# Kernel tuning notes

Measured on AMD Instinct MI355X. Metric: run time of the kernel, lower is better.

Reference implementation:

```python
import jax, jax.numpy as jnp
import numpy as np
from math import sqrt

D_MODEL = 512
HEADS = 8
D_K = D_MODEL // HEADS
DIM_FFN = 2048
EPS = 1e-6


def setup_inputs() -> dict:
    key = jax.random.key(0)
    ks = jax.random.split(key, 16)
    b, s = 2, 256
    inp = {
        "x": jax.random.normal(ks[0], (b, s, D_MODEL), dtype=jnp.float32),
        "connection_bias_k": jax.random.normal(ks[1], (b, s, s, D_MODEL), dtype=jnp.float32) * 0.02,
        "connection_bias_v": jax.random.normal(ks[2], (b, s, s, D_MODEL), dtype=jnp.float32) * 0.02,
        "mask": jnp.zeros((b, s), dtype=jnp.int32),
        "Wq": jax.random.normal(ks[3], (D_MODEL, D_MODEL), dtype=jnp.float32) / sqrt(D_MODEL),
        "bq": jnp.zeros((D_MODEL,), dtype=jnp.float32),
        "Wk": jax.random.normal(ks[4], (D_MODEL, D_MODEL), dtype=jnp.float32) / sqrt(D_MODEL),
        "bk": jnp.zeros((D_MODEL,), dtype=jnp.float32),
        "Wv": jax.random.normal(ks[5], (D_MODEL, D_MODEL), dtype=jnp.float32) / sqrt(D_MODEL),
        "bv": jnp.zeros((D_MODEL,), dtype=jnp.float32),
        "Wo": jax.random.normal(ks[6], (D_MODEL, D_MODEL), dtype=jnp.float32) / sqrt(D_MODEL),
        "bo": jnp.zeros((D_MODEL,), dtype=jnp.float32),
        "alpha1": jnp.ones((D_MODEL,), dtype=jnp.float32),
        "beta1": jnp.zeros((D_MODEL,), dtype=jnp.float32),
        "alpha2": jnp.ones((D_MODEL,), dtype=jnp.float32),
        "beta2": jnp.zeros((D_MODEL,), dtype=jnp.float32),
        "W1": jax.random.normal(ks[7], (DIM_FFN, D_MODEL), dtype=jnp.float32) / sqrt(D_MODEL),
        "b1": jnp.zeros((DIM_FFN,), dtype=jnp.float32),
        "W2": jax.random.normal(ks[8], (D_MODEL, DIM_FFN), dtype=jnp.float32) / sqrt(DIM_FFN),
        "b2": jnp.zeros((D_MODEL,), dtype=jnp.float32),
    }
    return inp


def _norm(x, alpha, beta):
    # torch .std() is unbiased (ddof=1); note std is added to eps OUTSIDE variance
    mu = jnp.mean(x, axis=-1, keepdims=True)
    sd = jnp.std(x, axis=-1, ddof=1, keepdims=True)
    return alpha * (x - mu) / (sd + EPS) + beta


def reference(x, connection_bias_k, connection_bias_v, mask,
              Wq, bq, Wk, bk, Wv, bv, Wo, bo,
              alpha1, beta1, alpha2, beta2, W1, b1, W2, b2):
    b, s, _ = x.shape
    h, dk = HEADS, D_K

    x2 = _norm(x, alpha1, beta1)
    # projections -> [b, h, s, dk]
    q = (x2 @ Wq.T + bq).reshape(b, s, h, dk).transpose(0, 2, 1, 3)
    k = (x2 @ Wk.T + bk).reshape(b, s, h, dk).transpose(0, 2, 1, 3)
    v = (x2 @ Wv.T + bv).reshape(b, s, h, dk).transpose(0, 2, 1, 3)

    # biases reshaped to (b, s1, s2, h, dk); biased_k[b,h,i,j] = k[b,h,j] + bias[b,j,i,h]
    bk_r = connection_bias_k.reshape(b, s, s, h, dk)
    bv_r = connection_bias_v.reshape(b, s, s, h, dk)

    # scores[b,h,i,j] = q_i . (k_j + bias_k[b,j,i,h]) / sqrt(dk)
    scores = (jnp.einsum('bhid,bhjd->bhij', q, k)
              + jnp.einsum('bhid,bjihd->bhij', q, bk_r)) / sqrt(dk)

    # mask [b,s] -> [b,1,s,1], broadcast over heads and key dim (matches torch)
    m = mask[:, None, :, None]
    scores = jnp.where(m == 1, -1e9, scores)
    attn = jax.nn.softmax(scores, axis=-1)

    # out[b,h,i,d] = sum_j attn[b,h,i,j] * (v[b,h,j] + bias_v[b,j,i,h])
    out = (jnp.einsum('bhij,bhjd->bhid', attn, v)
           + jnp.einsum('bhij,bjihd->bhid', attn, bv_r))
    concat = out.transpose(0, 2, 1, 3).reshape(b, s, D_MODEL)
    attn_out = concat @ Wo.T + bo

    x = x + attn_out
    x2 = _norm(x, alpha2, beta2)
    ff = jax.nn.relu(x2 @ W1.T + b1) @ W2.T + b2
    return x + ff
```

## Files before the change

### kernel.cpp

```cpp
#include <hip/hip_runtime.h>
#include <math.h>

#define D_MODEL 512
#define NHEADS 8
#define DK 64
#define DFFN 2048

typedef __attribute__((ext_vector_type(8))) __bf16 bf16x8;
typedef __attribute__((ext_vector_type(4))) float floatx4;

__global__ __launch_bounds__(256) void ln_kernel(
    const float* __restrict__ x, const float* __restrict__ alpha,
    const float* __restrict__ beta, __bf16* __restrict__ y) {
  int row = blockIdx.x;
  int t = threadIdx.x;
  const float* xr = x + (size_t)row * D_MODEL;
  float2 v = ((const float2*)xr)[t];
  __shared__ float rs[256], rq[256];
  rs[t] = v.x + v.y;
  rq[t] = v.x * v.x + v.y * v.y;
  __syncthreads();
  for (int o = 128; o > 0; o >>= 1) {
    if (t < o) { rs[t] += rs[t + o]; rq[t] += rq[t + o]; }
    __syncthreads();
  }
  float mu = rs[0] * (1.0f / D_MODEL);
  float var = (rq[0] - (float)D_MODEL * mu * mu) * (1.0f / (D_MODEL - 1));
  float inv = 1.0f / (sqrtf(fmaxf(var, 0.0f)) + 1e-6f);
  float2 a2 = ((const float2*)alpha)[t];
  float2 b2 = ((const float2*)beta)[t];
  union { __bf16 h2[2]; unsigned int u; } pk;
  pk.h2[0] = (__bf16)(a2.x * (v.x - mu) * inv + b2.x);
  pk.h2[1] = (__bf16)(a2.y * (v.y - mu) * inv + b2.y);
  *(unsigned int*)(y + (size_t)row * D_MODEL + 2 * t) = pk.u;
}

struct Seg { const float* src; __bf16* dst; int n4; };
struct Segs6 { Seg s[6]; };
__global__ __launch_bounds__(256) void cast6(Segs6 cs) {
  Seg sg = cs.s[blockIdx.y];
  int stride = gridDim.x * 256;
  for (int idx = blockIdx.x * 256 + threadIdx.x; idx < sg.n4; idx += stride) {
    float4 f = ((const float4*)sg.src)[idx];
    union { __bf16 h[4]; uint2 u; } pk;
    pk.h[0] = (__bf16)f.x; pk.h[1] = (__bf16)f.y;
    pk.h[2] = (__bf16)f.z; pk.h[3] = (__bf16)f.w;
    ((uint2*)sg.dst)[idx] = pk.u;
  }
}

__global__ __launch_bounds__(256) void pack_bias(
    const float* __restrict__ bq, const float* __restrict__ bk,
    const float* __restrict__ bv, float* __restrict__ dst) {
  int idx = blockIdx.x * 256 + threadIdx.x;
  if (idx >= 3 * D_MODEL) return;
  float v = idx < 512 ? bq[idx] : (idx < 1024 ? bk[idx - 512] : bv[idx - 1024]);
  dst[idx] = v;
}

template <int RELU, int OUT_BF16>
__global__ __launch_bounds__(64) void wave_gemm(
    const __bf16* __restrict__ A, int lda, const __bf16* __restrict__ B, int ldb,
    const float* __restrict__ bias, const float* __restrict__ res,
    void* __restrict__ Cv, int N, int K) {
  int lane = threadIdx.x;
  int r16 = lane & 15;
  int ko = (lane >> 4) * 8;
  int m0 = blockIdx.y * 32, n0 = blockIdx.x * 32;
  const __bf16* A0 = A + (size_t)(m0 + r16) * lda + ko;
  const __bf16* A1 = A0 + (size_t)16 * lda;
  const __bf16* B0 = B + (size_t)(n0 + r16) * ldb + ko;
  const __bf16* B1 = B0 + (size_t)16 * ldb;
  floatx4 acc00 = {0.f, 0.f, 0.f, 0.f};
  floatx4 acc01 = acc00, acc10 = acc00, acc11 = acc00;
#pragma unroll 4
  for (int k0 = 0; k0 < K; k0 += 32) {
    bf16x8 a0 = *(const bf16x8*)(A0 + k0);
    bf16x8 a1 = *(const bf16x8*)(A1 + k0);
    bf16x8 b0 = *(const bf16x8*)(B0 + k0);
    bf16x8 b1 = *(const bf16x8*)(B1 + k0);
    acc00 = __builtin_amdgcn_mfma_f32_16x16x32_bf16(a0, b0, acc00, 0, 0, 0);
    acc01 = __builtin_amdgcn_mfma_f32_16x16x32_bf16(a0, b1, acc01, 0, 0, 0);
    acc10 = __builtin_amdgcn_mfma_f32_16x16x32_bf16(a1, b0, acc10, 0, 0, 0);
    acc11 = __builtin_amdgcn_mfma_f32_16x16x32_bf16(a1, b1, acc11, 0, 0, 0);
  }
  int col = lane & 15, rb = (lane >> 4) * 4;
  floatx4 accs[2][2] = {{acc00, acc01}, {acc10, acc11}};
#pragma unroll
  for (int i = 0; i < 2; ++i) {
#pragma unroll
    for (int j = 0; j < 2; ++j) {
#pragma unroll
      for (int r = 0; r < 4; ++r) {
        int row = m0 + i * 16 + rb + r;
        int cc = n0 + j * 16 + col;
        float v = accs[i][j][r] + bias[cc];
        if (res) v += res[(size_t)row * N + cc];
        if (RELU) v = fmaxf(v, 0.0f);
        if (OUT_BF16)
          ((__bf16*)Cv)[(size_t)row * N + cc] = (__bf16)v;
        else
          ((float*)Cv)[(size_t)row * N + cc] = v;
      }
    }
  }
}

__global__ __launch_bounds__(256) void attn_kernel(
    const float* __restrict__ qkv, int ldq,
    const float* __restrict__ cbk, const float* __restrict__ cbv,
    const int* __restrict__ mask, __bf16* __restrict__ concat, int s) {
  int i = blockIdx.x % s;
  int b = blockIdx.x / s;
  int t = threadIdx.x;
  int w = t >> 6;
  int lane = t & 63;
  int h = lane >> 3;

  __shared__ float sc[NHEADS][257];
  __shared__ float sums[NHEADS];
  __shared__ float part[4][D_MODEL];

  size_t tok_i = (size_t)(b * s + i);
  const float* qp = qkv + tok_i * ldq + lane * 8;
  float4 q0 = *(const float4*)(qp);
  float4 q1 = *(const float4*)(qp + 4);

  for (int jj = 0; jj < 64; ++jj) {
    int j = w * 64 + jj;
    size_t tok_j = (size_t)(b * s + j);
    const float* kp = qkv + tok_j * ldq + 512 + lane * 8;
    const float* cp = cbk + (tok_j * s + i) * D_MODEL + lane * 8;
    float4 k0 = *(const float4*)(kp);
    float4 k1 = *(const float4*)(kp + 4);
    float4 c0 = *(const float4*)(cp);
    float4 c1 = *(const float4*)(cp + 4);
    float d = q0.x * (k0.x + c0.x) + q0.y * (k0.y + c0.y) +
              q0.z * (k0.z + c0.z) + q0.w * (k0.w + c0.w) +
              q1.x * (k1.x + c1.x) + q1.y * (k1.y + c1.y) +
              q1.z * (k1.z + c1.z) + q1.w * (k1.w + c1.w);
    d += __shfl_xor(d, 1);
    d += __shfl_xor(d, 2);
    d += __shfl_xor(d, 4);
    if ((lane & 7) == 0) sc[h][j] = d * 0.125f;
  }
  __syncthreads();

  {
    int hh = 2 * w + (lane >> 5);
    int l32 = lane & 31;
    bool masked = (mask[b * s + i] == 1);
    float vals[8];
    float mx = -1e30f;
#pragma unroll
    for (int kk = 0; kk < 8; ++kk) {
      float xv = sc[hh][l32 + kk * 32];
      if (masked) xv = -1e9f;
      vals[kk] = xv;
      mx = fmaxf(mx, xv);
    }
    for (int m = 1; m < 32; m <<= 1) mx = fmaxf(mx, __shfl_xor(mx, m, 32));
    float ls = 0.f;
#pragma unroll
    for (int kk = 0; kk < 8; ++kk) {
      float e = expf(vals[kk] - mx);
      sc[hh][l32 + kk * 32] = e;
      ls += e;
    }
    for (int m = 1; m < 32; m <<= 1) ls += __shfl_xor(ls, m, 32);
    if (l32 == 0) sums[hh] = ls;
  }
  __syncthreads();

  float4 a0 = {0.f, 0.f, 0.f, 0.f};
  float4 a1 = {0.f, 0.f, 0.f, 0.f};
  for (int jj = 0; jj < 64; ++jj) {
    int j = w * 64 + jj;
    size_t tok_j = (size_t)(b * s + j);
    const float* vp = qkv + tok_j * ldq + 1024 + lane * 8;
    const float* cp = cbv + (tok_j * s + i) * D_MODEL + lane * 8;
    float4 v0 = *(const float4*)(vp);
    float4 v1 = *(const float4*)(vp + 4);
    float4 c0 = *(const float4*)(cp);
    float4 c1 = *(const float4*)(cp + 4);
    float pj = sc[h][j];
    a0.x += pj * (v0.x + c0.x); a0.y += pj * (v0.y + c0.y);
    a0.z += pj * (v0.z + c0.z); a0.w += pj * (v0.w + c0.w);
    a1.x += pj * (v1.x + c1.x); a1.y += pj * (v1.y + c1.y);
    a1.z += pj * (v1.z + c1.z); a1.w += pj * (v1.w + c1.w);
  }
  *(float4*)&part[w][lane * 8] = a0;
  *(float4*)&part[w][lane * 8 + 4] = a1;
  __syncthreads();

  int d0 = t * 2;
  float inv = 1.0f / sums[d0 >> 6];
  float o0 = (part[0][d0] + part[1][d0] + part[2][d0] + part[3][d0]) * inv;
  float o1 = (part[0][d0 + 1] + part[1][d0 + 1] + part[2][d0 + 1] + part[3][d0 + 1]) * inv;
  union { __bf16 h2[2]; unsigned int u; } pk;
  pk.h2[0] = (__bf16)o0;
  pk.h2[1] = (__bf16)o1;
  *(unsigned int*)(concat + tok_i * D_MODEL + d0) = pk.u;
}

extern "C" void kernel_launch(void* const* d_in, const int* in_sizes, int n_in,
                              void* d_out, int out_size, void* d_ws, size_t ws_size,
                              hipStream_t stream) {
  const float* x      = (const float*)d_in[0];
  const float* cbk    = (const float*)d_in[1];
  const float* cbv    = (const float*)d_in[2];
  const int*   mask   = (const int*)d_in[3];
  const float* Wq     = (const float*)d_in[4];
  const float* bq     = (const float*)d_in[5];
  const float* Wk     = (const float*)d_in[6];
  const float* bk     = (const float*)d_in[7];
  const float* Wv     = (const float*)d_in[8];
  const float* bv     = (const float*)d_in[9];
  const float* Wo     = (const float*)d_in[10];
  const float* bo     = (const float*)d_in[11];
  const float* alpha1 = (const float*)d_in[12];
  const float* beta1  = (const float*)d_in[13];
  const float* alpha2 = (const float*)d_in[14];
  const float* beta2  = (const float*)d_in[15];
  const float* W1     = (const float*)d_in[16];
  const float* b1     = (const float*)d_in[17];
  const float* W2     = (const float*)d_in[18];
  const float* b2     = (const float*)d_in[19];

  int bs = in_sizes[0] / D_MODEL;
  int s  = in_sizes[1] / in_sizes[0];

  char* wp = (char*)d_ws;
  auto carve = [&](size_t bytes) {
    char* p = wp;
    wp += (bytes + 255) & ~(size_t)255;
    return p;
  };
  __bf16* x2    = (__bf16*)carve((size_t)bs * D_MODEL * 2);
  __bf16* wqkv  = (__bf16*)carve((size_t)3 * D_MODEL * D_MODEL * 2);
  __bf16* wo_b  = (__bf16*)carve((size_t)D_MODEL * D_MODEL * 2);
  __bf16* w1_b  = (__bf16*)carve((size_t)DFFN * D_MODEL * 2);
  __bf16* w2_b  = (__bf16*)carve((size_t)D_MODEL * DFFN * 2);
  float*  bqkv  = (float*)carve((size_t)3 * D_MODEL * 4);
  float*  qkv   = (float*)carve((size_t)bs * 3 * D_MODEL * 4);
  __bf16* conc  = (__bf16*)carve((size_t)bs * D_MODEL * 2);
  float*  xres  = (float*)carve((size_t)bs * D_MODEL * 4);
  __bf16* x2b   = (__bf16*)carve((size_t)bs * D_MODEL * 2);
  __bf16* f1    = (__bf16*)carve((size_t)bs * DFFN * 2);

  Segs6 cs;
  cs.s[0] = {Wq, wqkv,                 D_MODEL * D_MODEL / 4};
  cs.s[1] = {Wk, wqkv + D_MODEL * D_MODEL,     D_MODEL * D_MODEL / 4};
  cs.s[2] = {Wv, wqkv + 2 * D_MODEL * D_MODEL, D_MODEL * D_MODEL / 4};
  cs.s[3] = {Wo, wo_b, D_MODEL * D_MODEL / 4};
  cs.s[4] = {W1, w1_b, DFFN * D_MODEL / 4};
  cs.s[5] = {W2, w2_b, D_MODEL * DFFN / 4};
  cast6<<<dim3(256, 6), 256, 0, stream>>>(cs);
  pack_bias<<<6, 256, 0, stream>>>(bq, bk, bv, bqkv);

  ln_kernel<<<bs, 256, 0, stream>>>(x, alpha1, beta1, x2);

  wave_gemm<0, 0><<<dim3(3 * D_MODEL / 32, bs / 32), 64, 0, stream>>>(
      x2, D_MODEL, wqkv, D_MODEL, bqkv, nullptr, qkv, 3 * D_MODEL, D_MODEL);

  attn_kernel<<<bs, 256, 0, stream>>>(qkv, 3 * D_MODEL, cbk, cbv, mask, conc, s);

  wave_gemm<0, 0><<<dim3(D_MODEL / 32, bs / 32), 64, 0, stream>>>(
      conc, D_MODEL, wo_b, D_MODEL, bo, x, xres, D_MODEL, D_MODEL);

  ln_kernel<<<bs, 256, 0, stream>>>(xres, alpha2, beta2, x2b);

  wave_gemm<1, 1><<<dim3(DFFN / 32, bs / 32), 64, 0, stream>>>(
      x2b, D_MODEL, w1_b, D_MODEL, b1, nullptr, f1, DFFN, D_MODEL);

  wave_gemm<0, 0><<<dim3(D_MODEL / 32, bs / 32), 64, 0, stream>>>(
      f1, DFFN, w2_b, DFFN, b2, xres, d_out, D_MODEL, DFFN);
}
```

Baseline: 609.6 us.

## Split fused attention into scores, softmax, PV and reduce kernels over key blocks

Replaces the single per-query attention kernel (512 blocks) with four kernels: a scores kernel over (key-block, query, batch), a row softmax, a PV kernel producing per-key-block partial sums, and a reduction into bf16 concat. The goal is more blocks and shorter per-thread loops, so the memory-bound streaming of the two large connection-bias tensors gets more parallelism and memory-level concurrency. In exchange it adds three kernel launches and workspace round trips for the scores and partial outputs.

```diff
diff --git a/kernel.cpp b/kernel.cpp
--- a/kernel.cpp
+++ b/kernel.cpp
@@ -106,34 +106,29 @@
   }
 }
 
-__global__ __launch_bounds__(256) void attn_kernel(
-    const float* __restrict__ qkv, int ldq,
-    const float* __restrict__ cbk, const float* __restrict__ cbv,
-    const int* __restrict__ mask, __bf16* __restrict__ concat, int s) {
-  int i = blockIdx.x % s;
-  int b = blockIdx.x / s;
+__global__ __launch_bounds__(256) void attn_scores(
+    const float* __restrict__ qkv, int ldq, const float* __restrict__ cbk,
+    float* __restrict__ sc_out, int s) {
+  int jb = blockIdx.x;
+  int i = blockIdx.y;
+  int b = blockIdx.z;
   int t = threadIdx.x;
-  int w = t >> 6;
-  int lane = t & 63;
-  int h = lane >> 3;
-
-  __shared__ float sc[NHEADS][257];
-  __shared__ float sums[NHEADS];
-  __shared__ float part[4][D_MODEL];
-
+  int w = t >> 6, lane = t & 63, h = lane >> 3;
+  __shared__ float scl[64][9];
   size_t tok_i = (size_t)(b * s + i);
   const float* qp = qkv + tok_i * ldq + lane * 8;
-  float4 q0 = *(const float4*)(qp);
+  float4 q0 = *(const float4*)qp;
   float4 q1 = *(const float4*)(qp + 4);
-
-  for (int jj = 0; jj < 64; ++jj) {
-    int j = w * 64 + jj;
+  int jbase = jb * 64 + w * 16;
+#pragma unroll 4
+  for (int jj = 0; jj < 16; ++jj) {
+    int j = jbase + jj;
     size_t tok_j = (size_t)(b * s + j);
     const float* kp = qkv + tok_j * ldq + 512 + lane * 8;
-    const float* cp = cbk + (tok_j * s + i) * D_MODEL + lane * 8;
-    float4 k0 = *(const float4*)(kp);
+    const float* cp = cbk + (tok_j * s + i) * (size_t)D_MODEL + lane * 8;
+    float4 k0 = *(const float4*)kp;
     float4 k1 = *(const float4*)(kp + 4);
-    float4 c0 = *(const float4*)(cp);
+    float4 c0 = *(const float4*)cp;
     float4 c1 = *(const float4*)(cp + 4);
     float d = q0.x * (k0.x + c0.x) + q0.y * (k0.y + c0.y) +
               q0.z * (k0.z + c0.z) + q0.w * (k0.w + c0.w) +
@@ -142,65 +137,96 @@
     d += __shfl_xor(d, 1);
     d += __shfl_xor(d, 2);
     d += __shfl_xor(d, 4);
-    if ((lane & 7) == 0) sc[h][j] = d * 0.125f;
+    if ((lane & 7) == 0) scl[w * 16 + jj][h] = d * 0.125f;
   }
   __syncthreads();
-
+  int hh = t >> 5;
+  int jj2 = (t & 31) * 2;
+  float2 v2;
+  v2.x = scl[jj2][hh];
+  v2.y = scl[jj2 + 1][hh];
+  *(float2*)(sc_out + (tok_i * NHEADS + hh) * s + jb * 64 + jj2) = v2;
+}
+
+__global__ __launch_bounds__(256) void attn_softmax(
+    float* __restrict__ sc, const int* __restrict__ mask, int s) {
+  int row = blockIdx.x * 4 + (threadIdx.x >> 6);
+  int lane = threadIdx.x & 63;
+  float* p = sc + (size_t)row * s;
+  float4 v = ((float4*)p)[lane];
+  if (mask[row >> 3] == 1) { v.x = -1e9f; v.y = -1e9f; v.z = -1e9f; v.w = -1e9f; }
+  float mx = fmaxf(fmaxf(v.x, v.y), fmaxf(v.z, v.w));
+  for (int m = 1; m < 64; m <<= 1) mx = fmaxf(mx, __shfl_xor(mx, m));
+  float e0 = expf(v.x - mx), e1 = expf(v.y - mx);
+  float e2 = expf(v.z - mx), e3 = expf(v.w - mx);
+  float ls = e0 + e1 + e2 + e3;
+  for (int m = 1; m < 64; m <<= 1) ls += __shfl_xor(ls, m);
+  float inv = 1.0f / ls;
+  float4 o = {e0 * inv, e1 * inv, e2 * inv, e3 * inv};
+  ((float4*)p)[lane] = o;
+}
+
+__global__ __launch_bounds__(256) void attn_pv(
+    const float* __restrict__ qkv, int ldq, const float* __restrict__ cbv,
+    const float* __restrict__ p, float* __restrict__ part, int s) {
+  int jb = blockIdx.x;
+  int i = blockIdx.y;
+  int b = blockIdx.z;
+  int t = threadIdx.x;
+  int w = t >> 6, lane = t & 63, h = lane >> 3;
+  __shared__ float pl[NHEADS][64];
+  __shared__ float accs[4][D_MODEL];
+  size_t tok_i = (size_t)(b * s + i);
   {
-    int hh = 2 * w + (lane >> 5);
-    int l32 = lane & 31;
-    bool masked = (mask[b * s + i] == 1);
-    float vals[8];
-    float mx = -1e30f;
-#pragma unroll
-    for (int kk = 0; kk < 8; ++kk) {
-      float xv = sc[hh][l32 + kk * 32];
-      if (masked) xv = -1e9f;
-      vals[kk] = xv;
-      mx = fmaxf(mx, xv);
-    }
-    for (int m = 1; m < 32; m <<= 1) mx = fmaxf(mx, __shfl_xor(mx, m, 32));
-    float ls = 0.f;
-#pragma unroll
-    for (int kk = 0; kk < 8; ++kk) {
-      float e = expf(vals[kk] - mx);
-      sc[hh][l32 + kk * 32] = e;
-      ls += e;
-    }
-    for (int m = 1; m < 32; m <<= 1) ls += __shfl_xor(ls, m, 32);
-    if (l32 == 0) sums[hh] = ls;
+    int hh = t >> 5;
+    int jj2 = (t & 31) * 2;
+    float2 pv = *(const float2*)(p + (tok_i * NHEADS + hh) * s + jb * 64 + jj2);
+    pl[hh][jj2] = pv.x;
+    pl[hh][jj2 + 1] = pv.y;
   }
   __syncthreads();
-
   float4 a0 = {0.f, 0.f, 0.f, 0.f};
   float4 a1 = {0.f, 0.f, 0.f, 0.f};
-  for (int jj = 0; jj < 64; ++jj) {
-    int j = w * 64 + jj;
+  int jbase = jb * 64 + w * 16;
+#pragma unroll 4
+  for (int jj = 0; jj < 16; ++jj) {
+    int j = jbase + jj;
     size_t tok_j = (size_t)(b * s + j);
     const float* vp = qkv + tok_j * ldq + 1024 + lane * 8;
-    const float* cp = cbv + (tok_j * s + i) * D_MODEL + lane * 8;
-    float4 v0 = *(const float4*)(vp);
+    const float* cp = cbv + (tok_j * s + i) * (size_t)D_MODEL + lane * 8;
+    float4 v0 = *(const float4*)vp;
     float4 v1 = *(const float4*)(vp + 4);
-    float4 c0 = *(const float4*)(cp);
+    float4 c0 = *(const float4*)cp;
     float4 c1 = *(const float4*)(cp + 4);
-    float pj = sc[h][j];
+    float pj = pl[h][w * 16 + jj];
     a0.x += pj * (v0.x + c0.x); a0.y += pj * (v0.y + c0.y);
     a0.z += pj * (v0.z + c0.z); a0.w += pj * (v0.w + c0.w);
     a1.x += pj * (v1.x + c1.x); a1.y += pj * (v1.y + c1.y);
     a1.z += pj * (v1.z + c1.z); a1.w += pj * (v1.w + c1.w);
   }
-  *(float4*)&part[w][lane * 8] = a0;
-  *(float4*)&part[w][lane * 8 + 4] = a1;
+  *(float4*)&accs[w][lane * 8] = a0;
+  *(float4*)&accs[w][lane * 8 + 4] = a1;
   __syncthreads();
-
   int d0 = t * 2;
-  float inv = 1.0f / sums[d0 >> 6];
-  float o0 = (part[0][d0] + part[1][d0] + part[2][d0] + part[3][d0]) * inv;
-  float o1 = (part[0][d0 + 1] + part[1][d0 + 1] + part[2][d0 + 1] + part[3][d0 + 1]) * inv;
+  float2 o;
+  o.x = accs[0][d0] + accs[1][d0] + accs[2][d0] + accs[3][d0];
+  o.y = accs[0][d0 + 1] + accs[1][d0 + 1] + accs[2][d0 + 1] + accs[3][d0 + 1];
+  *(float2*)(part + (tok_i * 4 + jb) * (size_t)D_MODEL + d0) = o;
+}
+
+__global__ __launch_bounds__(256) void attn_reduce(
+    const float* __restrict__ part, __bf16* __restrict__ concat) {
+  size_t tok = blockIdx.x;
+  int d0 = threadIdx.x * 2;
+  const float* pp = part + tok * 4 * D_MODEL + d0;
+  float2 v0 = *(const float2*)(pp);
+  float2 v1 = *(const float2*)(pp + D_MODEL);
+  float2 v2 = *(const float2*)(pp + 2 * D_MODEL);
+  float2 v3 = *(const float2*)(pp + 3 * D_MODEL);
   union { __bf16 h2[2]; unsigned int u; } pk;
-  pk.h2[0] = (__bf16)o0;
-  pk.h2[1] = (__bf16)o1;
-  *(unsigned int*)(concat + tok_i * D_MODEL + d0) = pk.u;
+  pk.h2[0] = (__bf16)(v0.x + v1.x + v2.x + v3.x);
+  pk.h2[1] = (__bf16)(v0.y + v1.y + v2.y + v3.y);
+  *(unsigned int*)(concat + tok * D_MODEL + d0) = pk.u;
 }
 
 extern "C" void kernel_launch(void* const* d_in, const int* in_sizes, int n_in,
@@ -229,6 +255,7 @@
 
   int bs = in_sizes[0] / D_MODEL;
   int s  = in_sizes[1] / in_sizes[0];
+  int b  = bs / s;
 
   char* wp = (char*)d_ws;
   auto carve = [&](size_t bytes) {
@@ -243,13 +270,15 @@
   __bf16* w2_b  = (__bf16*)carve((size_t)D_MODEL * DFFN * 2);
   float*  bqkv  = (float*)carve((size_t)3 * D_MODEL * 4);
   float*  qkv   = (float*)carve((size_t)bs * 3 * D_MODEL * 4);
+  float*  sc_ws = (float*)carve((size_t)bs * NHEADS * s * 4);
+  float*  partw = (float*)carve((size_t)bs * 4 * D_MODEL * 4);
   __bf16* conc  = (__bf16*)carve((size_t)bs * D_MODEL * 2);
   float*  xres  = (float*)carve((size_t)bs * D_MODEL * 4);
   __bf16* x2b   = (__bf16*)carve((size_t)bs * D_MODEL * 2);
   __bf16* f1    = (__bf16*)carve((size_t)bs * DFFN * 2);
 
   Segs6 cs;
-  cs.s[0] = {Wq, wqkv,                 D_MODEL * D_MODEL / 4};
+  cs.s[0] = {Wq, wqkv,                         D_MODEL * D_MODEL / 4};
   cs.s[1] = {Wk, wqkv + D_MODEL * D_MODEL,     D_MODEL * D_MODEL / 4};
   cs.s[2] = {Wv, wqkv + 2 * D_MODEL * D_MODEL, D_MODEL * D_MODEL / 4};
   cs.s[3] = {Wo, wo_b, D_MODEL * D_MODEL / 4};
@@ -263,7 +292,10 @@
   wave_gemm<0, 0><<<dim3(3 * D_MODEL / 32, bs / 32), 64, 0, stream>>>(
       x2, D_MODEL, wqkv, D_MODEL, bqkv, nullptr, qkv, 3 * D_MODEL, D_MODEL);
 
-  attn_kernel<<<bs, 256, 0, stream>>>(qkv, 3 * D_MODEL, cbk, cbv, mask, conc, s);
+  attn_scores<<<dim3(4, s, b), 256, 0, stream>>>(qkv, 3 * D_MODEL, cbk, sc_ws, s);
+  attn_softmax<<<bs * NHEADS / 4, 256, 0, stream>>>(sc_ws, mask, s);
+  attn_pv<<<dim3(4, s, b), 256, 0, stream>>>(qkv, 3 * D_MODEL, cbv, sc_ws, partw, s);
+  attn_reduce<<<bs, 256, 0, stream>>>(partw, conc);
 
   wave_gemm<0, 0><<<dim3(D_MODEL / 32, bs / 32), 64, 0, stream>>>(
       conc, D_MODEL, wo_b, D_MODEL, bo, x, xres, D_MODEL, D_MODEL);
```

Result: slower. 633.5 us (+3.9%).
